# Kernel optimization log

Hardware: AMD Instinct MI355X
Metric: run time of the kernel (lower is better)

Reference implementation:

```python
import jax, jax.numpy as jnp
import numpy as np

NI = 256        # in_channels
QK = NI // 8    # query/key channels = 32
BS, H, W = 4, 64, 64


def setup_inputs() -> dict:
    key = jax.random.key(0)
    ks = jax.random.split(key, 8)
    x = jax.random.normal(ks[0], (BS, NI, H, W), dtype=jnp.float32)
    # 1x1 conv weights stored as [out_ch, in_ch] (kernel is 1x1)
    wq = jax.random.normal(ks[1], (QK, NI), dtype=jnp.float32) * (1.0 / np.sqrt(NI))
    bq = jnp.zeros((QK,), dtype=jnp.float32)
    wk = jax.random.normal(ks[2], (QK, NI), dtype=jnp.float32) * (1.0 / np.sqrt(NI))
    bk = jnp.zeros((QK,), dtype=jnp.float32)
    wv = jax.random.normal(ks[3], (NI, NI), dtype=jnp.float32) * (1.0 / np.sqrt(NI))
    bv = jnp.zeros((NI,), dtype=jnp.float32)
    # gamma is zero-init in the module; use small random values so the
    # attention branch actually contributes (post-training state).
    gamma = jax.random.normal(ks[4], (1, NI, 1, 1), dtype=jnp.float32) * 0.1
    return {"x": x, "wq": wq, "bq": bq, "wk": wk, "bk": bk,
            "wv": wv, "bv": bv, "gamma": gamma}


def reference(x, wq, bq, wk, bk, wv, bv, gamma):
    bs, c, h, w = x.shape
    n = h * w
    xf = x.reshape(bs, c, n)                       # [bs, c, N]
    # 1x1 convs == per-pixel linear maps over channels
    q = jnp.einsum('oc,bcn->bno', wq, xf) + bq     # [bs, N, qk]
    k = jnp.einsum('oc,bcn->bon', wk, xf) + bk[None, :, None]  # [bs, qk, N]
    v = jnp.einsum('oc,bcn->bon', wv, xf) + bv[None, :, None]  # [bs, c, N]
    attn = jax.nn.softmax(jnp.einsum('bnq,bqm->bnm', q, k), axis=-1)  # [bs, N, N]
    out = jnp.einsum('bcm,bnm->bcn', v, attn)      # value @ attn^T
    out = out.reshape(bs, c, h, w)
    return gamma * out + x
```

## Files before the change

kernel.cpp:

```cpp
#include <hip/hip_runtime.h>
#include <cstdint>
#include <cstddef>

#define NI   256
#define QKC  32
#define BS   4
#define NPIX 4096
#define LOG2E 1.4426950408889634f

typedef __bf16 bf16x8 __attribute__((ext_vector_type(8)));
typedef __bf16 bf16x4 __attribute__((ext_vector_type(4)));
typedef float  f32x16 __attribute__((ext_vector_type(16)));

__device__ inline f32x16 zero16() {
    f32x16 z;
    #pragma unroll
    for (int i = 0; i < 16; ++i) z[i] = 0.f;
    return z;
}

__global__ __launch_bounds__(256) void wconv_pack(
    const float* __restrict__ wq, const float* __restrict__ wk,
    const float* __restrict__ wv, __bf16* __restrict__ wpk)
{
    int f = blockIdx.x * 256 + threadIdx.x;
    int otl = f >> 10, rem = f & 1023;
    int kk = rem >> 6, h = (rem >> 5) & 1, l31 = rem & 31;
    int och = otl * 32 + l31, c0 = kk * 16 + 8 * h;
    const float* src = och < 32 ? wq + och * NI + c0
                     : och < 64 ? wk + (och - 32) * NI + c0
                                : wv + (och - 64) * NI + c0;
    float4 x0 = *(const float4*)src;
    float4 x1 = *(const float4*)(src + 4);
    __align__(16) __bf16 o8[8] = {
        (__bf16)x0.x, (__bf16)x0.y, (__bf16)x0.z, (__bf16)x0.w,
        (__bf16)x1.x, (__bf16)x1.y, (__bf16)x1.z, (__bf16)x1.w};
    *(uint4*)(wpk + (size_t)f * 8) = *(const uint4*)o8;
}

__global__ __launch_bounds__(256) void qkv_mfma(
    const float* __restrict__ x, const __bf16* __restrict__ wpk,
    const float* __restrict__ bq, const float* __restrict__ bk,
    const float* __restrict__ bv,
    __bf16* __restrict__ qpk, __bf16* __restrict__ kpk, __bf16* __restrict__ vpk)
{
    __shared__ __align__(16) __bf16 xT[32][264];
    __shared__ float bls[320];

    const int t = threadIdx.x, w = t >> 6, lane = t & 63;
    const int l31 = lane & 31, h = lane >> 5;
    const int b = blockIdx.y, n0 = blockIdx.x * 32, kt = blockIdx.x;

    for (int i = t; i < 320; i += 256)
        bls[i] = i < 32 ? bq[i] : i < 64 ? bk[i - 32] : bv[i - 64];

    {
        int n4 = (t & 7) * 4, cb = (t >> 3) * 8;
        float4 xv[8];
        #pragma unroll
        for (int j = 0; j < 8; ++j)
            xv[j] = *(const float4*)(x + ((size_t)(b * NI) + cb + j) * NPIX + n0 + n4);
        #pragma unroll
        for (int i = 0; i < 4; ++i) {
            __align__(16) __bf16 r8[8];
            #pragma unroll
            for (int j = 0; j < 8; ++j) r8[j] = (__bf16)((&xv[j].x)[i]);
            *(uint4*)&xT[n4 + i][cb] = *(const uint4*)r8;
        }
    }
    __syncthreads();

    f32x16 acc[3] = {zero16(), zero16(), zero16()};
    #pragma unroll 4
    for (int kk = 0; kk < 16; ++kk) {
        bf16x8 xf = *(const bf16x8*)&xT[l31][kk * 16 + 8 * h];
        #pragma unroll
        for (int jj = 0; jj < 3; ++jj) {
            int otl = w + 4 * jj;
            if (otl < 10) {
                bf16x8 wf = *(const bf16x8*)(wpk + (size_t)((otl * 16 + kk) * 64 + 32 * h + l31) * 8);
                acc[jj] = __builtin_amdgcn_mfma_f32_32x32x16_bf16(wf, xf, acc[jj], 0, 0, 0);
            }
        }
    }
    __syncthreads();

    __bf16 (*vT)[264] = xT;
    #pragma unroll
    for (int jj = 0; jj < 3; ++jj) {
        int otl = w + 4 * jj;
        if (otl >= 2 && otl < 10) {
            #pragma unroll
            for (int qd = 0; qd < 4; ++qd) {
                int c0v = (otl - 2) * 32 + 8 * qd + 4 * h;
                __align__(8) __bf16 q4[4];
                #pragma unroll
                for (int i = 0; i < 4; ++i)
                    q4[i] = (__bf16)(acc[jj][4 * qd + i] + bls[64 + c0v + i]);
                *(uint2*)&vT[l31][c0v] = *(const uint2*)q4;
            }
        }
    }
    #pragma unroll
    for (int jj = 0; jj < 3; ++jj) {
        int otl = w + 4 * jj;
        if (otl == 0) {
            #pragma unroll
            for (int kc = 0; kc < 2; ++kc) {
                __align__(16) __bf16 hi8[8], lo8[8];
                #pragma unroll
                for (int j = 0; j < 8; ++j) {
                    int r = 8 * kc + j;
                    int och = (r & 3) + 8 * (r >> 2) + 4 * h;
                    float val = (acc[jj][r] + bls[och]) * LOG2E;
                    __bf16 hh = (__bf16)val;
                    hi8[j] = hh;
                    lo8[j] = (__bf16)(val - (float)hh);
                }
                size_t base = ((((size_t)(b * 128 + kt) * 2 + 0) * 2 + kc) * 2 + h) * 32 + l31;
                *(uint4*)(qpk + base * 8) = *(const uint4*)hi8;
                size_t basel = ((((size_t)(b * 128 + kt) * 2 + 1) * 2 + kc) * 2 + h) * 32 + l31;
                *(uint4*)(qpk + basel * 8) = *(const uint4*)lo8;
            }
        } else if (otl == 1) {
            #pragma unroll
            for (int kc = 0; kc < 2; ++kc) {
                __align__(16) __bf16 k8[8];
                #pragma unroll
                for (int j = 0; j < 8; ++j) {
                    int r = 8 * kc + j;
                    int och = (r & 3) + 8 * (r >> 2) + 4 * h;
                    k8[j] = (__bf16)(acc[jj][r] + bls[32 + och]);
                }
                size_t base = (((size_t)(b * 128 + kt) * 2 + kc) * 2 + h) * 32 + l31;
                *(uint4*)(kpk + base * 8) = *(const uint4*)k8;
            }
        }
    }
    __syncthreads();

    #pragma unroll
    for (int kc = 0; kc < 2; ++kc)
        #pragma unroll
        for (int hh = 0; hh < 2; ++hh) {
            __align__(16) __bf16 f8[8];
            #pragma unroll
            for (int j = 0; j < 8; ++j) f8[j] = vT[16 * kc + 8 * hh + j][t];
            size_t base = (((size_t)(b * 128 + kt) * 2 + kc) * 2 + hh) * 256 + t;
            *(uint4*)(vpk + base * 8) = *(const uint4*)f8;
        }
}

__global__ __launch_bounds__(256) void attn_mfma(
    const __bf16* __restrict__ qpk, const __bf16* __restrict__ kpk,
    const __bf16* __restrict__ vpk,
    __bf16* __restrict__ Opart, float* __restrict__ dpart)
{
    __shared__ __align__(16) __bf16 pt_s[2][64][72];
    __shared__ float dwave[4][32];

    const int t = threadIdx.x;
    const int b = blockIdx.z, ksp = blockIdx.y;
    const int n0 = blockIdx.x * 64;
    const int w = t >> 6, lane = t & 63, l31 = lane & 31, h = lane >> 5;
    const int sr = w & 1, sc = w >> 1;
    const int kt0 = ksp * 64;

    const int qt = 2 * blockIdx.x + sr;
    bf16x8 qf[2][2];
    #pragma unroll
    for (int hl = 0; hl < 2; ++hl)
        #pragma unroll
        for (int kc = 0; kc < 2; ++kc)
            qf[hl][kc] = *(const bf16x8*)(qpk +
                (((((size_t)(b * 128 + qt) * 2 + hl) * 2 + kc) * 2 + h) * 32 + l31) * 8);

    auto kload = [&](int ktile, int kc) {
        return *(const bf16x8*)(kpk +
            ((((size_t)(b * 128 + ktile) * 2 + kc) * 2 + h) * 32 + l31) * 8);
    };

    f32x16 a00 = zero16(), a01 = zero16(), a10 = zero16(), a11 = zero16();
    float dacc = 0.f;

    auto sblock = [&](bf16x8 kh0, bf16x8 kh1, int buf) {
        f32x16 s = zero16();
        s = __builtin_amdgcn_mfma_f32_32x32x16_bf16(kh0, qf[0][0], s, 0, 0, 0);
        s = __builtin_amdgcn_mfma_f32_32x32x16_bf16(kh1, qf[0][1], s, 0, 0, 0);
        s = __builtin_amdgcn_mfma_f32_32x32x16_bf16(kh0, qf[1][0], s, 0, 0, 0);
        s = __builtin_amdgcn_mfma_f32_32x32x16_bf16(kh1, qf[1][1], s, 0, 0, 0);
        #pragma unroll
        for (int qd = 0; qd < 4; ++qd) {
            __align__(8) __bf16 e4[4];
            #pragma unroll
            for (int i = 0; i < 4; ++i) {
                float e = __builtin_amdgcn_exp2f(s[4 * qd + i]);
                dacc += e;
                e4[i] = (__bf16)e;
            }
            *(uint2*)&pt_s[buf][32 * sr + l31][32 * sc + 8 * qd + 4 * h] = *(const uint2*)e4;
        }
    };

    bf16x8 kh0 = kload(kt0 + sc, 0), kh1 = kload(kt0 + sc, 1);
    sblock(kh0, kh1, 0);
    kh0 = kload(kt0 + 2 + sc, 0); kh1 = kload(kt0 + 2 + sc, 1);
    __syncthreads();

    for (int mt = 0; mt < 32; ++mt) {
        const int cur = mt & 1;

        bf16x8 vf[2][2][2];
        #pragma unroll
        for (int i = 0; i < 2; ++i)
            #pragma unroll
            for (int kc = 0; kc < 2; ++kc)
                #pragma unroll
                for (int ctl = 0; ctl < 2; ++ctl)
                    vf[i][kc][ctl] = *(const bf16x8*)(vpk +
                        ((((size_t)(b * 128 + kt0 + 2 * mt + i) * 2 + kc) * 2 + h) * 256
                         + 64 * w + 32 * ctl + l31) * 8);

        if (mt < 31) {
            bf16x8 k0 = kh0, k1 = kh1;
            if (mt < 30) {
                kh0 = kload(kt0 + 2 * (mt + 2) + sc, 0);
                kh1 = kload(kt0 + 2 * (mt + 2) + sc, 1);
            }
            sblock(k0, k1, 1 - cur);
        }

        #pragma unroll
        for (int i = 0; i < 2; ++i)
            #pragma unroll
            for (int kc = 0; kc < 2; ++kc) {
                int col = 32 * i + 16 * kc + 8 * h;
                bf16x8 pa0 = *(const bf16x8*)&pt_s[cur][l31][col];
                bf16x8 pa1 = *(const bf16x8*)&pt_s[cur][32 + l31][col];
                a00 = __builtin_amdgcn_mfma_f32_32x32x16_bf16(pa0, vf[i][kc][0], a00, 0, 0, 0);
                a10 = __builtin_amdgcn_mfma_f32_32x32x16_bf16(pa1, vf[i][kc][0], a10, 0, 0, 0);
                a01 = __builtin_amdgcn_mfma_f32_32x32x16_bf16(pa0, vf[i][kc][1], a01, 0, 0, 0);
                a11 = __builtin_amdgcn_mfma_f32_32x32x16_bf16(pa1, vf[i][kc][1], a11, 0, 0, 0);
            }
        __syncthreads();
    }

    float dtot = dacc + __shfl_xor(dacc, 32);
    if (lane < 32) dwave[w][l31] = dtot;
    __syncthreads();
    if (w < 2 && lane < 32) {
        size_t dbase = ((size_t)(ksp * BS + b)) * NPIX + n0 + 32 * w;
        dpart[dbase + l31] = dwave[w][l31] + dwave[w + 2][l31];
    }

    size_t obase = (((size_t)(ksp * BS + b)) * NI + 64 * w + l31) * NPIX + n0;
    #pragma unroll
    for (int rq = 0; rq < 4; ++rq) {
        int nn = 8 * rq + 4 * h;
        __align__(8) __bf16 t00[4], t10[4], t01[4], t11[4];
        #pragma unroll
        for (int i = 0; i < 4; ++i) {
            t00[i] = (__bf16)a00[4 * rq + i];
            t10[i] = (__bf16)a10[4 * rq + i];
            t01[i] = (__bf16)a01[4 * rq + i];
            t11[i] = (__bf16)a11[4 * rq + i];
        }
        *(uint2*)(Opart + obase + nn)                          = *(const uint2*)t00;
        *(uint2*)(Opart + obase + 32 + nn)                     = *(const uint2*)t10;
        *(uint2*)(Opart + obase + (size_t)32 * NPIX + nn)      = *(const uint2*)t01;
        *(uint2*)(Opart + obase + (size_t)32 * NPIX + 32 + nn) = *(const uint2*)t11;
    }
}

__global__ __launch_bounds__(256) void combine(
    const float* __restrict__ x, const float* __restrict__ gamma,
    const __bf16* __restrict__ Opart, const float* __restrict__ dpart,
    float* __restrict__ out)
{
    int idx = (blockIdx.x * 256 + threadIdx.x) * 4;
    int n = idx & (NPIX - 1);
    int c = (idx >> 12) & (NI - 1);
    int b = idx >> 20;

    size_t o0 = (((size_t)(0 * BS + b)) * NI + c) * NPIX + n;
    size_t o1 = (((size_t)(1 * BS + b)) * NI + c) * NPIX + n;
    bf16x4 p0 = *(const bf16x4*)(Opart + o0);
    bf16x4 p1 = *(const bf16x4*)(Opart + o1);
    float4 da = *(const float4*)(dpart + ((size_t)(0 * BS + b)) * NPIX + n);
    float4 db = *(const float4*)(dpart + ((size_t)(1 * BS + b)) * NPIX + n);
    size_t xb = ((size_t)(b * NI) + c) * NPIX + n;
    float4 xv = *(const float4*)(x + xb);
    float g = gamma[c];

    float4 r;
    r.x = g * (((float)p0[0] + (float)p1[0]) / (da.x + db.x)) + xv.x;
    r.y = g * (((float)p0[1] + (float)p1[1]) / (da.y + db.y)) + xv.y;
    r.z = g * (((float)p0[2] + (float)p1[2]) / (da.z + db.z)) + xv.z;
    r.w = g * (((float)p0[3] + (float)p1[3]) / (da.w + db.w)) + xv.w;
    *(float4*)(out + xb) = r;
}

extern "C" void kernel_launch(void* const* d_in, const int* in_sizes, int n_in,
                              void* d_out, int out_size, void* d_ws, size_t ws_size,
                              hipStream_t stream)
{
    const float* x     = (const float*)d_in[0];
    const float* wq    = (const float*)d_in[1];
    const float* bq    = (const float*)d_in[2];
    const float* wk    = (const float*)d_in[3];
    const float* bk    = (const float*)d_in[4];
    const float* wv    = (const float*)d_in[5];
    const float* bv    = (const float*)d_in[6];
    const float* gamma = (const float*)d_in[7];
    float* out = (float*)d_out;

    const size_t WPK = (size_t)10240 * 8;
    const size_t QPK = (size_t)BS * 128 * 2 * 2 * 2 * 32 * 8;
    const size_t KPK = (size_t)BS * 128 * 2 * 2 * 32 * 8;
    const size_t VPK = (size_t)BS * 128 * 2 * 2 * 256 * 8;
    const size_t OSZ = (size_t)2 * BS * NI * NPIX;
    __bf16* wpk   = (__bf16*)d_ws;
    __bf16* qpk   = wpk + WPK;
    __bf16* kpk   = qpk + QPK;
    __bf16* vpk   = kpk + KPK;
    __bf16* Opart = vpk + VPK;
    float*  dpart = (float*)(Opart + OSZ);

    wconv_pack<<<dim3(40), 256, 0, stream>>>(wq, wk, wv, wpk);
    qkv_mfma<<<dim3(NPIX / 32, BS), 256, 0, stream>>>(x, wpk, bq, bk, bv, qpk, kpk, vpk);
    attn_mfma<<<dim3(64, 2, BS), 256, 0, stream>>>(qpk, kpk, vpk, Opart, dpart);
    combine<<<dim3(BS * NI * NPIX / 1024), 256, 0, stream>>>(x, gamma, Opart, dpart, out);
}
```

Before: 166.6 us.

## Split attention key range four ways and raise wave priority around MFMA blocks

Templates the attention kernel on the number of key-range splits. When the workspace is large enough it launches 4 splits instead of 2, doubling the grid from 512 to 1024 blocks for better CU occupancy, and the combine kernel sums the partial outputs and denominators. It also wraps the MFMA sections in s_setprio so waves issuing matrix ops get scheduling priority. The cost is twice the bf16 partial-output traffic written and re-read by the combine pass, plus shorter per-block loops with relatively more prologue overhead.

```diff
diff --git a/kernel.cpp b/kernel.cpp
--- a/kernel.cpp
+++ b/kernel.cpp
@@ -151,11 +151,13 @@
         }
 }
 
+template <int KSPLIT>
 __global__ __launch_bounds__(256) void attn_mfma(
     const __bf16* __restrict__ qpk, const __bf16* __restrict__ kpk,
     const __bf16* __restrict__ vpk,
     __bf16* __restrict__ Opart, float* __restrict__ dpart)
 {
+    constexpr int MT = 64 / KSPLIT;
     __shared__ __align__(16) __bf16 pt_s[2][64][72];
     __shared__ float dwave[4][32];
 
@@ -164,7 +166,7 @@
     const int n0 = blockIdx.x * 64;
     const int w = t >> 6, lane = t & 63, l31 = lane & 31, h = lane >> 5;
     const int sr = w & 1, sc = w >> 1;
-    const int kt0 = ksp * 64;
+    const int kt0 = ksp * (128 / KSPLIT);
 
     const int qt = 2 * blockIdx.x + sr;
     bf16x8 qf[2][2];
@@ -185,10 +187,12 @@
 
     auto sblock = [&](bf16x8 kh0, bf16x8 kh1, int buf) {
         f32x16 s = zero16();
+        __builtin_amdgcn_s_setprio(1);
         s = __builtin_amdgcn_mfma_f32_32x32x16_bf16(kh0, qf[0][0], s, 0, 0, 0);
         s = __builtin_amdgcn_mfma_f32_32x32x16_bf16(kh1, qf[0][1], s, 0, 0, 0);
         s = __builtin_amdgcn_mfma_f32_32x32x16_bf16(kh0, qf[1][0], s, 0, 0, 0);
         s = __builtin_amdgcn_mfma_f32_32x32x16_bf16(kh1, qf[1][1], s, 0, 0, 0);
+        __builtin_amdgcn_s_setprio(0);
         #pragma unroll
         for (int qd = 0; qd < 4; ++qd) {
             __align__(8) __bf16 e4[4];
@@ -207,7 +211,7 @@
     kh0 = kload(kt0 + 2 + sc, 0); kh1 = kload(kt0 + 2 + sc, 1);
     __syncthreads();
 
-    for (int mt = 0; mt < 32; ++mt) {
+    for (int mt = 0; mt < MT; ++mt) {
         const int cur = mt & 1;
 
         bf16x8 vf[2][2][2];
@@ -221,15 +225,16 @@
                         ((((size_t)(b * 128 + kt0 + 2 * mt + i) * 2 + kc) * 2 + h) * 256
                          + 64 * w + 32 * ctl + l31) * 8);
 
-        if (mt < 31) {
+        if (mt < MT - 1) {
             bf16x8 k0 = kh0, k1 = kh1;
-            if (mt < 30) {
+            if (mt < MT - 2) {
                 kh0 = kload(kt0 + 2 * (mt + 2) + sc, 0);
                 kh1 = kload(kt0 + 2 * (mt + 2) + sc, 1);
             }
             sblock(k0, k1, 1 - cur);
         }
 
+        __builtin_amdgcn_s_setprio(1);
         #pragma unroll
         for (int i = 0; i < 2; ++i)
             #pragma unroll
@@ -242,6 +247,7 @@
                 a01 = __builtin_amdgcn_mfma_f32_32x32x16_bf16(pa0, vf[i][kc][1], a01, 0, 0, 0);
                 a11 = __builtin_amdgcn_mfma_f32_32x32x16_bf16(pa1, vf[i][kc][1], a11, 0, 0, 0);
             }
+        __builtin_amdgcn_s_setprio(0);
         __syncthreads();
     }
 
@@ -272,6 +278,7 @@
     }
 }
 
+template <int KSPLIT>
 __global__ __launch_bounds__(256) void combine(
     const float* __restrict__ x, const float* __restrict__ gamma,
     const __bf16* __restrict__ Opart, const float* __restrict__ dpart,
@@ -282,21 +289,26 @@
     int c = (idx >> 12) & (NI - 1);
     int b = idx >> 20;
 
-    size_t o0 = (((size_t)(0 * BS + b)) * NI + c) * NPIX + n;
-    size_t o1 = (((size_t)(1 * BS + b)) * NI + c) * NPIX + n;
-    bf16x4 p0 = *(const bf16x4*)(Opart + o0);
-    bf16x4 p1 = *(const bf16x4*)(Opart + o1);
-    float4 da = *(const float4*)(dpart + ((size_t)(0 * BS + b)) * NPIX + n);
-    float4 db = *(const float4*)(dpart + ((size_t)(1 * BS + b)) * NPIX + n);
+    float4 osum = {0.f, 0.f, 0.f, 0.f};
+    float4 dsum = {0.f, 0.f, 0.f, 0.f};
+    #pragma unroll
+    for (int p = 0; p < KSPLIT; ++p) {
+        bf16x4 pp = *(const bf16x4*)(Opart + (((size_t)(p * BS + b)) * NI + c) * NPIX + n);
+        float4 dd = *(const float4*)(dpart + ((size_t)(p * BS + b)) * NPIX + n);
+        osum.x += (float)pp[0]; osum.y += (float)pp[1];
+        osum.z += (float)pp[2]; osum.w += (float)pp[3];
+        dsum.x += dd.x; dsum.y += dd.y; dsum.z += dd.z; dsum.w += dd.w;
+    }
+
     size_t xb = ((size_t)(b * NI) + c) * NPIX + n;
     float4 xv = *(const float4*)(x + xb);
     float g = gamma[c];
 
     float4 r;
-    r.x = g * (((float)p0[0] + (float)p1[0]) / (da.x + db.x)) + xv.x;
-    r.y = g * (((float)p0[1] + (float)p1[1]) / (da.y + db.y)) + xv.y;
-    r.z = g * (((float)p0[2] + (float)p1[2]) / (da.z + db.z)) + xv.z;
-    r.w = g * (((float)p0[3] + (float)p1[3]) / (da.w + db.w)) + xv.w;
+    r.x = g * (osum.x / dsum.x) + xv.x;
+    r.y = g * (osum.y / dsum.y) + xv.y;
+    r.z = g * (osum.z / dsum.z) + xv.z;
+    r.w = g * (osum.w / dsum.w) + xv.w;
     *(float4*)(out + xb) = r;
 }
 
@@ -318,16 +330,26 @@
     const size_t QPK = (size_t)BS * 128 * 2 * 2 * 2 * 32 * 8;
     const size_t KPK = (size_t)BS * 128 * 2 * 2 * 32 * 8;
     const size_t VPK = (size_t)BS * 128 * 2 * 2 * 256 * 8;
-    const size_t OSZ = (size_t)2 * BS * NI * NPIX;
     __bf16* wpk   = (__bf16*)d_ws;
     __bf16* qpk   = wpk + WPK;
     __bf16* kpk   = qpk + QPK;
     __bf16* vpk   = kpk + KPK;
     __bf16* Opart = vpk + VPK;
-    float*  dpart = (float*)(Opart + OSZ);
 
     wconv_pack<<<dim3(40), 256, 0, stream>>>(wq, wk, wv, wpk);
     qkv_mfma<<<dim3(NPIX / 32, BS), 256, 0, stream>>>(x, wpk, bq, bk, bv, qpk, kpk, vpk);
-    attn_mfma<<<dim3(64, 2, BS), 256, 0, stream>>>(qpk, kpk, vpk, Opart, dpart);
-    combine<<<dim3(BS * NI * NPIX / 1024), 256, 0, stream>>>(x, gamma, Opart, dpart, out);
-}
+
+    const size_t OSZ4  = (size_t)4 * BS * NI * NPIX;
+    const size_t need4 = (WPK + QPK + KPK + VPK + OSZ4) * sizeof(__bf16)
+                       + (size_t)4 * BS * NPIX * sizeof(float);
+    if (ws_size >= need4) {
+        float* dpart = (float*)(Opart + OSZ4);
+        attn_mfma<4><<<dim3(64, 4, BS), 256, 0, stream>>>(qpk, kpk, vpk, Opart, dpart);
+        combine<4><<<dim3(BS * NI * NPIX / 1024), 256, 0, stream>>>(x, gamma, Opart, dpart, out);
+    } else {
+        const size_t OSZ2 = (size_t)2 * BS * NI * NPIX;
+        float* dpart = (float*)(Opart + OSZ2);
+        attn_mfma<2><<<dim3(64, 2, BS), 256, 0, stream>>>(qpk, kpk, vpk, Opart, dpart);
+        combine<2><<<dim3(BS * NI * NPIX / 1024), 256, 0, stream>>>(x, gamma, Opart, dpart, out);
+    }
+}
```

Measured after the change: 160.3 us. 1.04x faster.

## Split attention value channels across two blocks and raise MFMA priority

Applied to the files above, without the earlier changes.

Each attention block now covers only 128 of the 256 output channels. The grid's y dimension doubles, so every wave keeps two accumulators instead of four and the launch bound asks for four blocks per CU. The aim is higher occupancy and more blocks to spread across CUs. In exchange, the QK^T scores and the exponentials are recomputed twice for every channel half. The change also wraps the MFMA sections in s_setprio.

```diff
diff --git a/kernel.cpp b/kernel.cpp
--- a/kernel.cpp
+++ b/kernel.cpp
@@ -151,20 +151,23 @@
         }
 }
 
-__global__ __launch_bounds__(256) void attn_mfma(
+__global__ __launch_bounds__(256, 4) void attn_mfma(
     const __bf16* __restrict__ qpk, const __bf16* __restrict__ kpk,
     const __bf16* __restrict__ vpk,
     __bf16* __restrict__ Opart, float* __restrict__ dpart)
 {
+    constexpr int MT = 32;
     __shared__ __align__(16) __bf16 pt_s[2][64][72];
     __shared__ float dwave[4][32];
 
     const int t = threadIdx.x;
-    const int b = blockIdx.z, ksp = blockIdx.y;
+    const int b = blockIdx.z;
+    const int ksp = blockIdx.y >> 1, cs = blockIdx.y & 1;
     const int n0 = blockIdx.x * 64;
     const int w = t >> 6, lane = t & 63, l31 = lane & 31, h = lane >> 5;
     const int sr = w & 1, sc = w >> 1;
     const int kt0 = ksp * 64;
+    const int cbase = 128 * cs + 32 * w + l31;
 
     const int qt = 2 * blockIdx.x + sr;
     bf16x8 qf[2][2];
@@ -179,16 +182,20 @@
         return *(const bf16x8*)(kpk +
             ((((size_t)(b * 128 + ktile) * 2 + kc) * 2 + h) * 32 + l31) * 8);
     };
-
-    f32x16 a00 = zero16(), a01 = zero16(), a10 = zero16(), a11 = zero16();
+    const __bf16* vbase = vpk +
+        ((((size_t)(b * 128 + kt0) * 2) * 2 + h) * 256 + cbase) * 8;
+
+    f32x16 a0 = zero16(), a1 = zero16();
     float dacc = 0.f;
 
     auto sblock = [&](bf16x8 kh0, bf16x8 kh1, int buf) {
         f32x16 s = zero16();
+        __builtin_amdgcn_s_setprio(1);
         s = __builtin_amdgcn_mfma_f32_32x32x16_bf16(kh0, qf[0][0], s, 0, 0, 0);
         s = __builtin_amdgcn_mfma_f32_32x32x16_bf16(kh1, qf[0][1], s, 0, 0, 0);
         s = __builtin_amdgcn_mfma_f32_32x32x16_bf16(kh0, qf[1][0], s, 0, 0, 0);
         s = __builtin_amdgcn_mfma_f32_32x32x16_bf16(kh1, qf[1][1], s, 0, 0, 0);
+        __builtin_amdgcn_s_setprio(0);
         #pragma unroll
         for (int qd = 0; qd < 4; ++qd) {
             __align__(8) __bf16 e4[4];
@@ -207,29 +214,27 @@
     kh0 = kload(kt0 + 2 + sc, 0); kh1 = kload(kt0 + 2 + sc, 1);
     __syncthreads();
 
-    for (int mt = 0; mt < 32; ++mt) {
+    for (int mt = 0; mt < MT; ++mt) {
         const int cur = mt & 1;
 
-        bf16x8 vf[2][2][2];
+        bf16x8 vf[2][2];
         #pragma unroll
         for (int i = 0; i < 2; ++i)
             #pragma unroll
             for (int kc = 0; kc < 2; ++kc)
-                #pragma unroll
-                for (int ctl = 0; ctl < 2; ++ctl)
-                    vf[i][kc][ctl] = *(const bf16x8*)(vpk +
-                        ((((size_t)(b * 128 + kt0 + 2 * mt + i) * 2 + kc) * 2 + h) * 256
-                         + 64 * w + 32 * ctl + l31) * 8);
-
-        if (mt < 31) {
+                vf[i][kc] = *(const bf16x8*)(vbase +
+                    ((size_t)(2 * mt + i) * 2 + kc) * (2 * 256 * 8));
+
+        if (mt < MT - 1) {
             bf16x8 k0 = kh0, k1 = kh1;
-            if (mt < 30) {
+            if (mt < MT - 2) {
                 kh0 = kload(kt0 + 2 * (mt + 2) + sc, 0);
                 kh1 = kload(kt0 + 2 * (mt + 2) + sc, 1);
             }
             sblock(k0, k1, 1 - cur);
         }
 
+        __builtin_amdgcn_s_setprio(1);
         #pragma unroll
         for (int i = 0; i < 2; ++i)
             #pragma unroll
@@ -237,38 +242,33 @@
                 int col = 32 * i + 16 * kc + 8 * h;
                 bf16x8 pa0 = *(const bf16x8*)&pt_s[cur][l31][col];
                 bf16x8 pa1 = *(const bf16x8*)&pt_s[cur][32 + l31][col];
-                a00 = __builtin_amdgcn_mfma_f32_32x32x16_bf16(pa0, vf[i][kc][0], a00, 0, 0, 0);
-                a10 = __builtin_amdgcn_mfma_f32_32x32x16_bf16(pa1, vf[i][kc][0], a10, 0, 0, 0);
-                a01 = __builtin_amdgcn_mfma_f32_32x32x16_bf16(pa0, vf[i][kc][1], a01, 0, 0, 0);
-                a11 = __builtin_amdgcn_mfma_f32_32x32x16_bf16(pa1, vf[i][kc][1], a11, 0, 0, 0);
-            }
+                a0 = __builtin_amdgcn_mfma_f32_32x32x16_bf16(pa0, vf[i][kc], a0, 0, 0, 0);
+                a1 = __builtin_amdgcn_mfma_f32_32x32x16_bf16(pa1, vf[i][kc], a1, 0, 0, 0);
+            }
+        __builtin_amdgcn_s_setprio(0);
         __syncthreads();
     }
 
     float dtot = dacc + __shfl_xor(dacc, 32);
     if (lane < 32) dwave[w][l31] = dtot;
     __syncthreads();
-    if (w < 2 && lane < 32) {
+    if (cs == 0 && w < 2 && lane < 32) {
         size_t dbase = ((size_t)(ksp * BS + b)) * NPIX + n0 + 32 * w;
         dpart[dbase + l31] = dwave[w][l31] + dwave[w + 2][l31];
     }
 
-    size_t obase = (((size_t)(ksp * BS + b)) * NI + 64 * w + l31) * NPIX + n0;
+    size_t obase = (((size_t)(ksp * BS + b)) * NI + cbase) * NPIX + n0;
     #pragma unroll
     for (int rq = 0; rq < 4; ++rq) {
         int nn = 8 * rq + 4 * h;
-        __align__(8) __bf16 t00[4], t10[4], t01[4], t11[4];
+        __align__(8) __bf16 t0[4], t1[4];
         #pragma unroll
         for (int i = 0; i < 4; ++i) {
-            t00[i] = (__bf16)a00[4 * rq + i];
-            t10[i] = (__bf16)a10[4 * rq + i];
-            t01[i] = (__bf16)a01[4 * rq + i];
-            t11[i] = (__bf16)a11[4 * rq + i];
-        }
-        *(uint2*)(Opart + obase + nn)                          = *(const uint2*)t00;
-        *(uint2*)(Opart + obase + 32 + nn)                     = *(const uint2*)t10;
-        *(uint2*)(Opart + obase + (size_t)32 * NPIX + nn)      = *(const uint2*)t01;
-        *(uint2*)(Opart + obase + (size_t)32 * NPIX + 32 + nn) = *(const uint2*)t11;
+            t0[i] = (__bf16)a0[4 * rq + i];
+            t1[i] = (__bf16)a1[4 * rq + i];
+        }
+        *(uint2*)(Opart + obase + nn)      = *(const uint2*)t0;
+        *(uint2*)(Opart + obase + 32 + nn) = *(const uint2*)t1;
     }
 }
 
@@ -328,6 +328,6 @@
 
     wconv_pack<<<dim3(40), 256, 0, stream>>>(wq, wk, wv, wpk);
     qkv_mfma<<<dim3(NPIX / 32, BS), 256, 0, stream>>>(x, wpk, bq, bk, bv, qpk, kpk, vpk);
-    attn_mfma<<<dim3(64, 2, BS), 256, 0, stream>>>(qpk, kpk, vpk, Opart, dpart);
+    attn_mfma<<<dim3(64, 4, BS), 256, 0, stream>>>(qpk, kpk, vpk, Opart, dpart);
     combine<<<dim3(BS * NI * NPIX / 1024), 256, 0, stream>>>(x, gamma, Opart, dpart, out);
 }
```

After: 161.1 us. 3.3% less time.
